# Performance work log

Measured on AMD Instinct MI355X. Metric: run time of the kernel, lower is better.

Reference implementation:

```python
import jax, jax.numpy as jnp
import numpy as np

N = 100000
E = 1600000
CIN = 32
COUT = 32
K = 5
EPS = 1e-15      # PyG GMMConv EPS in sigma^2 denominator
BN_EPS = 1e-5    # torch BatchNorm1d default eps


def gmm_conv(x, edge_index, edge_attr, g, mu, sigma, root, bias):
    """PyG GMMConv (MoNet), aggr='mean', root_weight=True, bias=True."""
    src, dst = edge_index[0], edge_index[1]
    n = x.shape[0]
    k = mu.shape[0]
    cout = root.shape[1]
    xg = (x @ g).reshape(n, k, cout)                # [N, K, out]
    xj = xg[src]                                    # gather: [E, K, out]
    d = edge_attr[:, None, :] - mu[None, :, :]      # [E, K, 3]
    w = jnp.exp(-0.5 * jnp.sum(d * d / (EPS + sigma[None] ** 2), axis=-1))  # [E, K]
    msg = jnp.einsum('eko,ek->eo', xj, w)           # [E, out]
    agg = jax.ops.segment_sum(msg, dst, num_segments=n)
    cnt = jax.ops.segment_sum(jnp.ones((msg.shape[0],), x.dtype), dst, num_segments=n)
    agg = agg / jnp.clip(cnt, 1.0)[:, None]         # mean aggregation
    return agg + x @ root + bias


def batch_norm(x, gamma, beta):
    # training-mode BatchNorm1d: biased batch statistics over node dim
    m = x.mean(0)
    v = x.var(0)
    return (x - m) * jax.lax.rsqrt(v + BN_EPS) * gamma + beta


def setup_inputs() -> dict:
    key = jax.random.key(0)
    ks = jax.random.split(key, 12)
    p = lambda k, s, sc=0.1: jax.random.normal(k, s, jnp.float32) * sc
    return {
        'x': jax.random.normal(ks[0], (N, CIN), jnp.float32),
        'edge_index': jax.random.randint(ks[1], (2, E), 0, N, jnp.int32),
        'edge_attr': jax.random.uniform(ks[2], (E, 3), jnp.float32),
        # left conv1: in -> out, K=5
        'g1': p(ks[3], (CIN, K * COUT)), 'mu1': p(ks[4], (K, 3), 1.0), 'sigma1': jnp.ones((K, 3), jnp.float32),
        'root1': p(ks[5], (CIN, COUT)), 'b1': jnp.zeros((COUT,), jnp.float32),
        'gam1': jnp.ones((COUT,), jnp.float32), 'bet1': jnp.zeros((COUT,), jnp.float32),
        # left conv2: out -> out, K=5
        'g2': p(ks[6], (COUT, K * COUT)), 'mu2': p(ks[7], (K, 3), 1.0), 'sigma2': jnp.ones((K, 3), jnp.float32),
        'root2': p(ks[8], (COUT, COUT)), 'b2': jnp.zeros((COUT,), jnp.float32),
        'gam2': jnp.ones((COUT,), jnp.float32), 'bet2': jnp.zeros((COUT,), jnp.float32),
        # shortcut conv: in -> out, K=1
        'gs': p(ks[9], (CIN, 1 * COUT)), 'mus': p(ks[10], (1, 3), 1.0), 'sigmas': jnp.ones((1, 3), jnp.float32),
        'roots': p(ks[11], (CIN, COUT)), 'bs': jnp.zeros((COUT,), jnp.float32),
        'gams': jnp.ones((COUT,), jnp.float32), 'bets': jnp.zeros((COUT,), jnp.float32),
    }


def reference(x, edge_index, edge_attr,
              g1, mu1, sigma1, root1, b1, gam1, bet1,
              g2, mu2, sigma2, root2, b2, gam2, bet2,
              gs, mus, sigmas, roots, bs, gams, bets):
    h = jax.nn.elu(batch_norm(gmm_conv(x, edge_index, edge_attr, g1, mu1, sigma1, root1, b1), gam1, bet1))
    h = batch_norm(gmm_conv(h, edge_index, edge_attr, g2, mu2, sigma2, root2, b2), gam2, bet2)
    s = batch_norm(gmm_conv(x, edge_index, edge_attr, gs, mus, sigmas, roots, bs), gams, bets)
    return jax.nn.elu(h + s)
```

## Files before the change

### kernel.cpp

```cpp
#include <hip/hip_runtime.h>
#include <hip/hip_bf16.h>
#include <math.h>


#define ELU(v) ((v) > 0.f ? (v) : (__expf(v) - 1.f))

using short8  = __attribute__((ext_vector_type(8))) short;
using floatx4 = __attribute__((ext_vector_type(4))) float;

__device__ inline ushort f2bf(float f) {
    __hip_bfloat16 h = __float2bfloat16(f);
    return *reinterpret_cast<ushort*>(&h);
}
__device__ inline float bflo(unsigned u) { return __uint_as_float(u << 16); }
__device__ inline float bfhi(unsigned u) { return __uint_as_float(u & 0xffff0000u); }
__device__ inline unsigned pack_bf2(float lo, float hi) {
    return ((unsigned)f2bf(hi) << 16) | (unsigned)f2bf(lo);
}

__global__ __launch_bounds__(256) void prep_xb(
    const float* __restrict__ x, unsigned* __restrict__ XB, int N)
{
    const int idx = blockIdx.x * blockDim.x + threadIdx.x;
    if (idx >= N * 16) return;
    const float2 p = ((const float2*)x)[idx];
    XB[idx] = pack_bf2(p.x, p.y);
}

__global__ __launch_bounds__(256) void prep_hxb(
    const float* __restrict__ out1, const float* __restrict__ coef,
    unsigned* __restrict__ XB, int N)
{
    const int idx = blockIdx.x * blockDim.x + threadIdx.x;
    if (idx >= N * 16) return;
    const int l = idx & 15;
    const float2 p = ((const float2*)out1)[idx];
    const int c0 = 2 * l, c1 = 2 * l + 1;
    float v0 = p.x * coef[c0] + coef[32 + c0];
    float v1 = p.y * coef[c1] + coef[32 + c1];
    v0 = ELU(v0); v1 = ELU(v1);
    XB[idx] = pack_bf2(v0, v1);
}

#define CH 4096
__global__ __launch_bounds__(256) void binfill_k(
    const int* __restrict__ ei, const float* __restrict__ attr,
    int* __restrict__ gcur, unsigned long long* __restrict__ pay0,
    int E, int NB, int CAPc)
{
    __shared__ unsigned long long srec[CH];
    __shared__ unsigned char sbin[CH];
    __shared__ int cnt[256], offs[256], wcur[256], gbase[256], sc[256];

    const int t = threadIdx.x;
    const int e0 = blockIdx.x * CH;
    const int nrec = min(CH, E - e0);

    cnt[t] = 0;
    __syncthreads();

    unsigned long long rec[16];
    int bin[16];
#pragma unroll
    for (int r = 0; r < 16; ++r) {
        const int e = e0 + r * 256 + t;
        bin[r] = -1;
        if (e < E) {
            const int s = ei[e], d = ei[E + e];
            const float a0 = attr[(size_t)e * 3 + 0];
            const float a1 = attr[(size_t)e * 3 + 1];
            const float a2 = attr[(size_t)e * 3 + 2];
            const unsigned q0 = (unsigned)min(max((int)(a0 * 4096.f), 0), 4095);
            const unsigned q1 = (unsigned)min(max((int)(a1 * 4096.f), 0), 4095);
            const unsigned q2 = (unsigned)min(max((int)(a2 * 4096.f), 0), 4095);
            rec[r] = (unsigned long long)(unsigned)s
                   | ((unsigned long long)(d & 511) << 17)
                   | ((unsigned long long)q0 << 26)
                   | ((unsigned long long)q1 << 38)
                   | ((unsigned long long)q2 << 50);
            bin[r] = d >> 9;
            atomicAdd(&cnt[bin[r]], 1);
        }
    }
    __syncthreads();

    const int v = cnt[t];
    sc[t] = v;
    __syncthreads();
    for (int o = 1; o < 256; o <<= 1) {
        const int xx = (t >= o) ? sc[t - o] : 0;
        __syncthreads();
        sc[t] += xx;
        __syncthreads();
    }
    offs[t] = sc[t] - v;
    wcur[t] = sc[t] - v;
    __syncthreads();

#pragma unroll
    for (int r = 0; r < 16; ++r) {
        if (bin[r] >= 0) {
            const int pos = atomicAdd(&wcur[bin[r]], 1);
            srec[pos] = rec[r];
            sbin[pos] = (unsigned char)bin[r];
        }
    }
    __syncthreads();

    if (t < NB && cnt[t] > 0) gbase[t] = atomicAdd(&gcur[t], cnt[t]);
    __syncthreads();

    for (int i = t; i < nrec; i += 256) {
        const int b = sbin[i];
        const int idx = gbase[b] + (i - offs[b]);
        if (idx < CAPc)
            pay0[(size_t)b * CAPc + idx] = srec[i];
    }
}

__global__ __launch_bounds__(256) void scatter2_k(
    const unsigned long long* __restrict__ pay0, const int* __restrict__ gcur,
    int* __restrict__ row_ptr, unsigned long long* __restrict__ pay,
    int N, int CAPc, int NB)
{
    const int b = blockIdx.x;
    const int t = threadIdx.x;
    const int d0 = b << 9;
    const int nd = min(512, N - d0);

    __shared__ int cnt[512];
    __shared__ int offs[512];
    __shared__ int sscan[256];
    __shared__ int ssum[256];

    ssum[t] = (t < b && t < NB) ? gcur[t] : 0;
    for (int i = t; i < 512; i += 256) cnt[i] = 0;
    __syncthreads();
    for (int o = 128; o > 0; o >>= 1) {
        if (t < o) ssum[t] += ssum[t + o];
        __syncthreads();
    }
    const int base = ssum[0];

    const int total = min(gcur[b], CAPc);
    const unsigned long long* src = pay0 + (size_t)b * CAPc;

    for (int i = t; i < total; i += 256) {
        const int dlo = (int)((src[i] >> 17) & 511);
        atomicAdd(&cnt[dlo], 1);
    }
    __syncthreads();

    const int c0 = cnt[2 * t], c1 = cnt[2 * t + 1];
    const int pairsum = c0 + c1;
    sscan[t] = pairsum;
    __syncthreads();
    for (int o = 1; o < 256; o <<= 1) {
        const int xx = (t >= o) ? sscan[t - o] : 0;
        __syncthreads();
        sscan[t] += xx;
        __syncthreads();
    }
    const int excl = sscan[t] - pairsum;
    offs[2 * t] = excl;
    offs[2 * t + 1] = excl + c0;
    __syncthreads();
    const int btotal = sscan[255];

    for (int i = t; i < nd; i += 256) row_ptr[d0 + i] = base + offs[i];
    if (b == NB - 1 && t == 0) row_ptr[N] = base + btotal;

    for (int i = t; i < 512; i += 256) cnt[i] = offs[i];
    __syncthreads();

    for (int i = t; i < total; i += 256) {
        const unsigned long long rec = src[i];
        const int dlo = (int)((rec >> 17) & 511);
        const int p = atomicAdd(&cnt[dlo], 1);
        pay[base + p] = rec;
    }
}

template <bool HAS_S>
__global__ __launch_bounds__(256) void gt_k(
    const unsigned* __restrict__ XB,
    const unsigned long long* __restrict__ payload,
    const int* __restrict__ row_ptr,
    const float* __restrict__ mu_m, const float* __restrict__ sg_m,
    const float* __restrict__ mu_s, const float* __restrict__ sg_s,
    const float* __restrict__ g,
    const float* __restrict__ rootm,
    const float* __restrict__ bm,
    const float* __restrict__ gss,
    const float* __restrict__ rootss,
    const float* __restrict__ bss,
    float* __restrict__ out_m, float* __restrict__ out_s,
    float* __restrict__ stats_m, float* __restrict__ stats_s,
    int N, int ntiles)
{
    constexpr int KS = HAS_S ? 6 : 5;
    constexpr int SLS = KS + 1;
    constexpr int STRIDE = SLS * 16 + 4;
    constexpr float DQ = 1.0f / 4096.0f;

    __shared__ float wbuf[16][17][8];
    __shared__ unsigned sA[16 * STRIDE];
    __shared__ float sred[128];

    const int tid = threadIdx.x;
    const int l = tid & 15, grp = tid >> 4;
    const int lane = tid & 63, l4 = lane & 15, quad = lane >> 4;
    const int wv = tid >> 6;
    const int half = wv & 1;

    const bool convRole = (wv < 2);
    const bool sRole = HAS_S && (wv >= 2);
    short8 Bf[6];
    float bias0 = 0.f;
    if (convRole) {
#pragma unroll
        for (int s = 0; s < 5; ++s)
#pragma unroll
            for (int j = 0; j < 8; ++j)
                Bf[s][j] = (short)f2bf(g[(quad * 8 + j) * 160 + s * 32 + 16 * half + l4]);
#pragma unroll
        for (int j = 0; j < 8; ++j)
            Bf[5][j] = (short)f2bf(rootm[(quad * 8 + j) * 32 + 16 * half + l4]);
        bias0 = bm[16 * half + l4];
    } else if (sRole) {
#pragma unroll
        for (int j = 0; j < 8; ++j) {
            Bf[0][j] = (short)f2bf(gss[(quad * 8 + j) * 32 + 16 * half + l4]);
            Bf[1][j] = (short)f2bf(rootss[(quad * 8 + j) * 32 + 16 * half + l4]);
        }
        bias0 = bss[16 * half + l4];
    }

    float mm[15], im[15];
#pragma unroll
    for (int i = 0; i < 15; ++i) {
        mm[i] = mu_m[i];
        float s = sg_m[i];
        im[i] = 1.0f / (1e-15f + s * s);
    }
    float ms[3], is[3];
    if (HAS_S) {
#pragma unroll
        for (int i = 0; i < 3; ++i) {
            ms[i] = mu_s[i];
            float s = sg_s[i];
            is[i] = 1.0f / (1e-15f + s * s);
        }
    }

    float ps = 0.f, pq = 0.f;

    for (int tile = blockIdx.x; tile < ntiles; tile += gridDim.x) {
        const int dst = tile * 16 + grp;
        float2 acc[KS];
#pragma unroll
        for (int k = 0; k < KS; ++k) acc[k] = make_float2(0.f, 0.f);

        int rp0 = 0, deg = 0;
        if (dst < N) { rp0 = row_ptr[dst]; deg = row_ptr[dst + 1] - rp0; }

        auto body = [&](int j) {
            const float4 a = *(const float4*)&wbuf[grp][j][0];
            const float4 b = *(const float4*)&wbuf[grp][j][4];
            const int sj = __float_as_int(a.x);
            const unsigned u = XB[(size_t)sj * 16 + l];
            const float x0 = bflo(u), x1 = bfhi(u);
            acc[0].x = fmaf(a.y, x0, acc[0].x); acc[0].y = fmaf(a.y, x1, acc[0].y);
            acc[1].x = fmaf(a.z, x0, acc[1].x); acc[1].y = fmaf(a.z, x1, acc[1].y);
            acc[2].x = fmaf(a.w, x0, acc[2].x); acc[2].y = fmaf(a.w, x1, acc[2].y);
            acc[3].x = fmaf(b.x, x0, acc[3].x); acc[3].y = fmaf(b.x, x1, acc[3].y);
            acc[4].x = fmaf(b.y, x0, acc[4].x); acc[4].y = fmaf(b.y, x1, acc[4].y);
            if (HAS_S) {
                acc[5].x = fmaf(b.z, x0, acc[5].x); acc[5].y = fmaf(b.z, x1, acc[5].y);
            }
        };

        for (int base = 0; base < deg; base += 16) {
            const int nj = min(16, deg - base);
            if (l < nj) {
                unsigned long long pq8 = payload[rp0 + base + l];
                const int src = (int)(pq8 & 0x1FFFFull);
                float p0 = ((int)((pq8 >> 26) & 0xFFF) + 0.5f) * DQ;
                float p1 = ((int)((pq8 >> 38) & 0xFFF) + 0.5f) * DQ;
                float p2 = ((int)((pq8 >> 50) & 0xFFF) + 0.5f) * DQ;
                float w[5], wS = 0.f;
#pragma unroll
                for (int k = 0; k < 5; ++k) {
                    float d0 = p0 - mm[k * 3 + 0];
                    float d1 = p1 - mm[k * 3 + 1];
                    float d2 = p2 - mm[k * 3 + 2];
                    float q = d0 * d0 * im[k * 3 + 0] + d1 * d1 * im[k * 3 + 1]
                            + d2 * d2 * im[k * 3 + 2];
                    w[k] = __expf(-0.5f * q);
                }
                if (HAS_S) {
                    float d0 = p0 - ms[0], d1 = p1 - ms[1], d2 = p2 - ms[2];
                    float q = d0 * d0 * is[0] + d1 * d1 * is[1] + d2 * d2 * is[2];
                    wS = __expf(-0.5f * q);
                }
                float4* wp = (float4*)&wbuf[grp][l][0];
                wp[0] = make_float4(__int_as_float(src), w[0], w[1], w[2]);
                wp[1] = make_float4(w[3], w[4], wS, 0.f);
            }
            int j = 0;
            for (; j + 3 < nj; j += 4) { body(j); body(j + 1); body(j + 2); body(j + 3); }
            for (; j < nj; ++j) body(j);
        }

        {
            unsigned* arow = sA + grp * STRIDE;
            const float invd = 1.0f / fmaxf((float)deg, 1.0f);
            const bool ok = (dst < N);
#pragma unroll
            for (int k = 0; k < KS; ++k)
                arow[k * 16 + l] = ok ? pack_bf2(acc[k].x * invd, acc[k].y * invd) : 0u;
            arow[KS * 16 + l] = ok ? XB[(size_t)dst * 16 + l] : 0u;
        }
        __syncthreads();

        if (convRole || sRole) {
            floatx4 C = {0.f, 0.f, 0.f, 0.f};
            if (convRole) {
#pragma unroll
                for (int s = 0; s < 6; ++s) {
                    const int slot = (s < 5) ? s : KS;
                    const uint4 av = *(const uint4*)(sA + l4 * STRIDE + slot * 16 + quad * 4);
                    const short8 A = *reinterpret_cast<const short8*>(&av);
                    C = __builtin_amdgcn_mfma_f32_16x16x32_bf16(A, Bf[s], C, 0, 0, 0);
                }
            } else {
#pragma unroll
                for (int s = 0; s < 2; ++s) {
                    const int slot = 5 + s;
                    const uint4 av = *(const uint4*)(sA + l4 * STRIDE + slot * 16 + quad * 4);
                    const short8 A = *reinterpret_cast<const short8*>(&av);
                    C = __builtin_amdgcn_mfma_f32_16x16x32_bf16(A, Bf[s], C, 0, 0, 0);
                }
            }

            float* outp = convRole ? out_m : out_s;
#pragma unroll
            for (int r = 0; r < 4; ++r) {
                const int n = tile * 16 + quad * 4 + r;
                if (n < N) {
                    const float v = C[r] + bias0;
                    outp[(size_t)n * 32 + 16 * half + l4] = v;
                    ps += v; pq += v * v;
                }
            }
        }
        __syncthreads();
    }

    if (tid < 128) sred[tid] = 0.f;
    __syncthreads();
    if (convRole) {
        atomicAdd(&sred[16 * half + l4], ps);
        atomicAdd(&sred[32 + 16 * half + l4], pq);
    } else if (sRole) {
        atomicAdd(&sred[64 + 16 * half + l4], ps);
        atomicAdd(&sred[96 + 16 * half + l4], pq);
    }
    __syncthreads();
    const int spread = (blockIdx.x & 7) * 64;
    if (tid < 64) atomicAdd(&stats_m[spread + tid], sred[tid]);
    else if (HAS_S && tid < 128) atomicAdd(&stats_s[spread + tid - 64], sred[tid]);
}

__global__ void coef2_k(const float* __restrict__ stats1, const float* __restrict__ gam1,
                        const float* __restrict__ bet1, float* __restrict__ coef1,
                        const float* __restrict__ stats2, const float* __restrict__ gam2,
                        const float* __restrict__ bet2, float* __restrict__ coef2,
                        float invN)
{
    const int t = threadIdx.x;
    const int set = t >> 6;
    const int c = t & 63;
    if (c >= 32) return;
    const float* stats = set ? stats2 : stats1;
    const float* gam = set ? gam2 : gam1;
    const float* bet = set ? bet2 : bet1;
    float* coef = set ? coef2 : coef1;
    if (set && !stats) return;
    float s = 0.f, q = 0.f;
    for (int p = 0; p < 8; ++p) { s += stats[p * 64 + c]; q += stats[p * 64 + 32 + c]; }
    float m = s * invN;
    float v = fmaxf(q * invN - m * m, 0.f);
    float sc = gam[c] * rsqrtf(v + 1e-5f);
    coef[c] = sc;
    coef[32 + c] = bet[c] - m * sc;
}

__global__ __launch_bounds__(256) void final_k(
    const float* __restrict__ o2, const float* __restrict__ os,
    const float* __restrict__ c2, const float* __restrict__ cs,
    float* __restrict__ out, int total)
{
    int idx = blockIdx.x * blockDim.x + threadIdx.x;
    if (idx >= total) return;
    int c = idx & 31;
    float v = o2[idx] * c2[c] + c2[32 + c] + os[idx] * cs[c] + cs[32 + c];
    out[idx] = ELU(v);
}

extern "C" void kernel_launch(void* const* d_in, const int* in_sizes, int n_in,
                              void* d_out, int out_size, void* d_ws, size_t ws_size,
                              hipStream_t stream)
{
    const float* x      = (const float*)d_in[0];
    const int*   ei     = (const int*)d_in[1];
    const float* attr   = (const float*)d_in[2];
    const float* g1     = (const float*)d_in[3];
    const float* mu1    = (const float*)d_in[4];
    const float* sig1   = (const float*)d_in[5];
    const float* root1  = (const float*)d_in[6];
    const float* b1     = (const float*)d_in[7];
    const float* gam1   = (const float*)d_in[8];
    const float* bet1   = (const float*)d_in[9];
    const float* g2     = (const float*)d_in[10];
    const float* mu2    = (const float*)d_in[11];
    const float* sig2   = (const float*)d_in[12];
    const float* root2  = (const float*)d_in[13];
    const float* b2     = (const float*)d_in[14];
    const float* gam2   = (const float*)d_in[15];
    const float* bet2   = (const float*)d_in[16];
    const float* gs     = (const float*)d_in[17];
    const float* mus    = (const float*)d_in[18];
    const float* sigs   = (const float*)d_in[19];
    const float* roots  = (const float*)d_in[20];
    const float* bs     = (const float*)d_in[21];
    const float* gams   = (const float*)d_in[22];
    const float* bets   = (const float*)d_in[23];

    const int N = in_sizes[0] / 32;
    const int E = in_sizes[1] / 2;
    const int total = N * 32;
    const int ntiles = (N + 15) / 16;
    const int NB = (N + 511) >> 9;
    const int CAPc = ((((E + NB - 1) / NB) * 5) / 4 + 15) & ~15;

    char* ws = (char*)d_ws;
    size_t off = 0;
    auto carve = [&](size_t bytes) {
        void* p = ws + off;
        off = (off + bytes + 255) & ~(size_t)255;
        return p;
    };
    unsigned* XB   = (unsigned*)carve((size_t)N * 16 * 4);
    float*  OUT1   = (float*)carve((size_t)N * 32 * 4);
    float*  OUT2   = (float*)carve((size_t)N * 32 * 4);
    float*  OUTS   = (float*)carve((size_t)N * 32 * 4);
    unsigned long long* PAY  = (unsigned long long*)carve((size_t)E * 8);
    unsigned long long* PAY0 = (unsigned long long*)carve((size_t)NB * CAPc * 8);
    int*    ROWP   = (int*)carve((size_t)(N + 1) * 4);
    int*    GCUR   = (int*)carve(256 * 4);
    float*  STATS  = (float*)carve(3 * 512 * 4);
    float*  COEF   = (float*)carve(3 * 64 * 4);
    float* stats1 = STATS, *stats2 = STATS + 512, *statsS = STATS + 1024;
    float* coef1 = COEF, *coef2 = COEF + 64, *coefS = COEF + 128;
    (void)ws_size; (void)n_in; (void)out_size;

    const float invN = 1.0f / (float)N;
    const int ew = (total + 255) / 256;
    const int epb = (N * 16 + 255) / 256;
    const int nfb = (E + CH - 1) / CH;
    const int gtb = ntiles < 2048 ? ntiles : 2048;

    hipMemsetAsync(GCUR, 0, 256 * 4, stream);
    hipMemsetAsync(STATS, 0, 3 * 512 * 4, stream);

    binfill_k<<<nfb, 256, 0, stream>>>(ei, attr, GCUR, PAY0, E, NB, CAPc);
    scatter2_k<<<NB, 256, 0, stream>>>(PAY0, GCUR, ROWP, PAY, N, CAPc, NB);

    prep_xb<<<epb, 256, 0, stream>>>(x, XB, N);
    gt_k<true><<<gtb, 256, 0, stream>>>(XB, PAY, ROWP,
        mu1, sig1, mus, sigs, g1, root1, b1, gs, roots, bs,
        OUT1, OUTS, stats1, statsS, N, ntiles);
    coef2_k<<<1, 128, 0, stream>>>(stats1, gam1, bet1, coef1,
                                   statsS, gams, bets, coefS, invN);

    prep_hxb<<<epb, 256, 0, stream>>>(OUT1, coef1, XB, N);
    gt_k<false><<<gtb, 256, 0, stream>>>(XB, PAY, ROWP,
        mu2, sig2, nullptr, nullptr, g2, root2, b2, nullptr, nullptr, nullptr,
        OUT2, nullptr, stats2, nullptr, N, ntiles);
    coef2_k<<<1, 128, 0, stream>>>(stats2, gam2, bet2, coef2,
                                   nullptr, nullptr, nullptr, nullptr, invN);

    final_k<<<ew, 256, 0, stream>>>(OUT2, OUTS, coef2, coefS, (float*)d_out, total);
}
```

Baseline: 317.4 us.

## Use atomic dynamic tile scheduling and batch neighbor gathers ahead of weight math

Replaces the static grid-stride tile loop with an atomic work counter, reset in scatter2_k, so blocks pull tiles on demand and balance uneven degrees. In the edge loop, all 16 neighbor feature loads are issued up front into registers before the Gaussian weights are computed, with inactive lanes masked to zero weight. This hides gather latency behind the exp math. The root feature load is also hoisted to the start of the tile. The cost is extra atomics and a __syncthreads per tile, wasted loads for partial chunks, and higher register pressure.

```diff
diff --git a/kernel.cpp b/kernel.cpp
--- a/kernel.cpp
+++ b/kernel.cpp
@@ -121,6 +121,7 @@
 __global__ __launch_bounds__(256) void scatter2_k(
     const unsigned long long* __restrict__ pay0, const int* __restrict__ gcur,
     int* __restrict__ row_ptr, unsigned long long* __restrict__ pay,
+    int* __restrict__ tctr,
     int N, int CAPc, int NB)
 {
     const int b = blockIdx.x;
@@ -132,6 +133,8 @@
     __shared__ int offs[512];
     __shared__ int sscan[256];
     __shared__ int ssum[256];
+
+    if (b == 0 && t == 0) { tctr[0] = 0; tctr[1] = 0; }
 
     ssum[t] = (t < b && t < NB) ? gcur[t] : 0;
     for (int i = t; i < 512; i += 256) cnt[i] = 0;
@@ -196,6 +199,7 @@
     const float* __restrict__ bss,
     float* __restrict__ out_m, float* __restrict__ out_s,
     float* __restrict__ stats_m, float* __restrict__ stats_s,
+    int* __restrict__ tilectr,
     int N, int ntiles)
 {
     constexpr int KS = HAS_S ? 6 : 5;
@@ -206,6 +210,7 @@
     __shared__ float wbuf[16][17][8];
     __shared__ unsigned sA[16 * STRIDE];
     __shared__ float sred[128];
+    __shared__ int stile;
 
     const int tid = threadIdx.x;
     const int l = tid & 15, grp = tid >> 4;
@@ -255,61 +260,79 @@
 
     float ps = 0.f, pq = 0.f;
 
-    for (int tile = blockIdx.x; tile < ntiles; tile += gridDim.x) {
+    for (;;) {
+        if (tid == 0) stile = atomicAdd(tilectr, 1);
+        __syncthreads();
+        const int tile = stile;
+        if (tile >= ntiles) break;
+
         const int dst = tile * 16 + grp;
         float2 acc[KS];
 #pragma unroll
         for (int k = 0; k < KS; ++k) acc[k] = make_float2(0.f, 0.f);
 
         int rp0 = 0, deg = 0;
-        if (dst < N) { rp0 = row_ptr[dst]; deg = row_ptr[dst + 1] - rp0; }
-
-        auto body = [&](int j) {
-            const float4 a = *(const float4*)&wbuf[grp][j][0];
-            const float4 b = *(const float4*)&wbuf[grp][j][4];
-            const int sj = __float_as_int(a.x);
-            const unsigned u = XB[(size_t)sj * 16 + l];
-            const float x0 = bflo(u), x1 = bfhi(u);
-            acc[0].x = fmaf(a.y, x0, acc[0].x); acc[0].y = fmaf(a.y, x1, acc[0].y);
-            acc[1].x = fmaf(a.z, x0, acc[1].x); acc[1].y = fmaf(a.z, x1, acc[1].y);
-            acc[2].x = fmaf(a.w, x0, acc[2].x); acc[2].y = fmaf(a.w, x1, acc[2].y);
-            acc[3].x = fmaf(b.x, x0, acc[3].x); acc[3].y = fmaf(b.x, x1, acc[3].y);
-            acc[4].x = fmaf(b.y, x0, acc[4].x); acc[4].y = fmaf(b.y, x1, acc[4].y);
-            if (HAS_S) {
-                acc[5].x = fmaf(b.z, x0, acc[5].x); acc[5].y = fmaf(b.z, x1, acc[5].y);
-            }
-        };
+        unsigned rootv = 0;
+        if (dst < N) {
+            rp0 = row_ptr[dst];
+            deg = row_ptr[dst + 1] - rp0;
+            rootv = XB[(size_t)dst * 16 + l];
+        }
 
         for (int base = 0; base < deg; base += 16) {
             const int nj = min(16, deg - base);
-            if (l < nj) {
-                unsigned long long pq8 = payload[rp0 + base + l];
-                const int src = (int)(pq8 & 0x1FFFFull);
-                float p0 = ((int)((pq8 >> 26) & 0xFFF) + 0.5f) * DQ;
-                float p1 = ((int)((pq8 >> 38) & 0xFFF) + 0.5f) * DQ;
-                float p2 = ((int)((pq8 >> 50) & 0xFFF) + 0.5f) * DQ;
-                float w[5], wS = 0.f;
-#pragma unroll
-                for (int k = 0; k < 5; ++k) {
-                    float d0 = p0 - mm[k * 3 + 0];
-                    float d1 = p1 - mm[k * 3 + 1];
-                    float d2 = p2 - mm[k * 3 + 2];
-                    float q = d0 * d0 * im[k * 3 + 0] + d1 * d1 * im[k * 3 + 1]
-                            + d2 * d2 * im[k * 3 + 2];
-                    w[k] = __expf(-0.5f * q);
+            const bool act = (l < nj);
+
+            unsigned long long pq8 = 0;
+            if (act) pq8 = payload[rp0 + base + l];
+            const int src = (int)(pq8 & 0x1FFFFull);
+            wbuf[grp][l][0] = __int_as_float(src);
+
+            unsigned xv[16];
+#pragma unroll
+            for (int j = 0; j < 16; ++j) {
+                const int sj = __float_as_int(wbuf[grp][j][0]);
+                xv[j] = XB[(size_t)sj * 16 + l];
+            }
+            __builtin_amdgcn_sched_barrier(0);
+
+            const float am = act ? 1.f : 0.f;
+            const float p0 = ((int)((pq8 >> 26) & 0xFFF) + 0.5f) * DQ;
+            const float p1 = ((int)((pq8 >> 38) & 0xFFF) + 0.5f) * DQ;
+            const float p2 = ((int)((pq8 >> 50) & 0xFFF) + 0.5f) * DQ;
+            float w[5], wS = 0.f;
+#pragma unroll
+            for (int k = 0; k < 5; ++k) {
+                const float d0 = p0 - mm[k * 3 + 0];
+                const float d1 = p1 - mm[k * 3 + 1];
+                const float d2 = p2 - mm[k * 3 + 2];
+                const float q = d0 * d0 * im[k * 3 + 0] + d1 * d1 * im[k * 3 + 1]
+                              + d2 * d2 * im[k * 3 + 2];
+                w[k] = __expf(-0.5f * q);
+            }
+            if (HAS_S) {
+                const float d0 = p0 - ms[0], d1 = p1 - ms[1], d2 = p2 - ms[2];
+                const float q = d0 * d0 * is[0] + d1 * d1 * is[1] + d2 * d2 * is[2];
+                wS = __expf(-0.5f * q);
+            }
+            float4* wp = (float4*)&wbuf[grp][l][0];
+            wp[0] = make_float4(__int_as_float(src), w[0] * am, w[1] * am, w[2] * am);
+            wp[1] = make_float4(w[3] * am, w[4] * am, wS * am, 0.f);
+
+#pragma unroll
+            for (int j = 0; j < 16; ++j) {
+                const float4 a = *(const float4*)&wbuf[grp][j][0];
+                const float4 b = *(const float4*)&wbuf[grp][j][4];
+                const float x0 = bflo(xv[j]), x1 = bfhi(xv[j]);
+                acc[0].x = fmaf(a.y, x0, acc[0].x); acc[0].y = fmaf(a.y, x1, acc[0].y);
+                acc[1].x = fmaf(a.z, x0, acc[1].x); acc[1].y = fmaf(a.z, x1, acc[1].y);
+                acc[2].x = fmaf(a.w, x0, acc[2].x); acc[2].y = fmaf(a.w, x1, acc[2].y);
+                acc[3].x = fmaf(b.x, x0, acc[3].x); acc[3].y = fmaf(b.x, x1, acc[3].y);
+                acc[4].x = fmaf(b.y, x0, acc[4].x); acc[4].y = fmaf(b.y, x1, acc[4].y);
+                if (HAS_S) {
+                    acc[5].x = fmaf(b.z, x0, acc[5].x); acc[5].y = fmaf(b.z, x1, acc[5].y);
                 }
-                if (HAS_S) {
-                    float d0 = p0 - ms[0], d1 = p1 - ms[1], d2 = p2 - ms[2];
-                    float q = d0 * d0 * is[0] + d1 * d1 * is[1] + d2 * d2 * is[2];
-                    wS = __expf(-0.5f * q);
-                }
-                float4* wp = (float4*)&wbuf[grp][l][0];
-                wp[0] = make_float4(__int_as_float(src), w[0], w[1], w[2]);
-                wp[1] = make_float4(w[3], w[4], wS, 0.f);
             }
-            int j = 0;
-            for (; j + 3 < nj; j += 4) { body(j); body(j + 1); body(j + 2); body(j + 3); }
-            for (; j < nj; ++j) body(j);
         }
 
         {
@@ -319,7 +342,7 @@
 #pragma unroll
             for (int k = 0; k < KS; ++k)
                 arow[k * 16 + l] = ok ? pack_bf2(acc[k].x * invd, acc[k].y * invd) : 0u;
-            arow[KS * 16 + l] = ok ? XB[(size_t)dst * 16 + l] : 0u;
+            arow[KS * 16 + l] = ok ? rootv : 0u;
         }
         __syncthreads();
 
@@ -461,6 +484,7 @@
     int*    GCUR   = (int*)carve(256 * 4);
     float*  STATS  = (float*)carve(3 * 512 * 4);
     float*  COEF   = (float*)carve(3 * 64 * 4);
+    int*    TCTR   = (int*)carve(2 * 4);
     float* stats1 = STATS, *stats2 = STATS + 512, *statsS = STATS + 1024;
     float* coef1 = COEF, *coef2 = COEF + 64, *coefS = COEF + 128;
     (void)ws_size; (void)n_in; (void)out_size;
@@ -475,19 +499,19 @@
     hipMemsetAsync(STATS, 0, 3 * 512 * 4, stream);
 
     binfill_k<<<nfb, 256, 0, stream>>>(ei, attr, GCUR, PAY0, E, NB, CAPc);
-    scatter2_k<<<NB, 256, 0, stream>>>(PAY0, GCUR, ROWP, PAY, N, CAPc, NB);
+    scatter2_k<<<NB, 256, 0, stream>>>(PAY0, GCUR, ROWP, PAY, TCTR, N, CAPc, NB);
 
     prep_xb<<<epb, 256, 0, stream>>>(x, XB, N);
     gt_k<true><<<gtb, 256, 0, stream>>>(XB, PAY, ROWP,
         mu1, sig1, mus, sigs, g1, root1, b1, gs, roots, bs,
-        OUT1, OUTS, stats1, statsS, N, ntiles);
+        OUT1, OUTS, stats1, statsS, TCTR + 0, N, ntiles);
     coef2_k<<<1, 128, 0, stream>>>(stats1, gam1, bet1, coef1,
                                    statsS, gams, bets, coefS, invN);
 
     prep_hxb<<<epb, 256, 0, stream>>>(OUT1, coef1, XB, N);
     gt_k<false><<<gtb, 256, 0, stream>>>(XB, PAY, ROWP,
         mu2, sig2, nullptr, nullptr, g2, root2, b2, nullptr, nullptr, nullptr,
-        OUT2, nullptr, stats2, nullptr, N, ntiles);
+        OUT2, nullptr, stats2, nullptr, TCTR + 1, N, ntiles);
     coef2_k<<<1, 128, 0, stream>>>(stats2, gam2, bet2, coef2,
                                    nullptr, nullptr, nullptr, nullptr, invN);
 
```

Measured after the change: 399.5 us. 25.9% more time.
